# Kernel optimization log

Measured on AMD Instinct MI355X. Metric: run time of the kernel, lower is better.

The kernel has to match this reference:

```python
import jax, jax.numpy as jnp
import numpy as np

B, H, E = 16, 4096, 512
N_MODES = 24  # len(index_q), permutation of range(48//2)


def setup_inputs() -> dict:
    key = jax.random.key(0)
    ks = jax.random.split(key, 7)
    s = 1.0 / np.sqrt(E)
    inp = {
        "x": jax.random.normal(ks[0], (B, H, E), jnp.float32),
        "Wq": jax.random.normal(ks[1], (E, E), jnp.float32) * s,
        "bq": jax.random.normal(ks[2], (E,), jnp.float32) * s,
        "Wk": jax.random.normal(ks[3], (E, E), jnp.float32) * s,
        "bk": jax.random.normal(ks[4], (E,), jnp.float32) * s,
        "Wv": jax.random.normal(ks[5], (E, E), jnp.float32) * s,
        "bv": jax.random.normal(ks[6], (E,), jnp.float32) * s,
        # shuffled permutation of range(24), as in the module __init__
        "index_q": jnp.asarray(np.random.RandomState(0).permutation(N_MODES), jnp.int32),
    }
    return inp


def reference(x, Wq, bq, Wk, bk, Wv, bv, index_q):
    # nn.Linear: y = x @ W.T + b
    Q = x @ Wq.T + bq
    K = x @ Wk.T + bk
    V = x @ Wv.T + bv  # computed but unused downstream (faithful to original bug)
    del V

    # rFFT over feature dim, gather selected frequency modes (vectorized,
    # replacing the original per-index Python loops)
    xq_ft = jnp.fft.rfft(Q, axis=-1)[:, :, index_q]          # [B,H,24] complex
    xk_ft = jnp.fft.rfft(K, axis=-1)[:, :, index_q]          # [B,H,24]
    xv_ft = xk_ft                                            # original uses rfft(K) for V too

    # cross-frequency attention: contract over H (no conjugation, as torch.einsum)
    xqk_ft = jnp.einsum('bhx,bhy->bxy', xq_ft, xk_ft)        # [B,24,24] complex
    att = jax.nn.softmax(jnp.abs(xqk_ft), axis=-1)           # real [B,24,24]
    att_c = jax.lax.complex(att, jnp.zeros_like(att))
    xqkv_ft = jnp.einsum('bxy,bhy->bhx', att_c, xv_ft)       # [B,H,24]

    # scatter selected modes back into the full spectrum, inverse rFFT
    n_freq = E // 2 + 1
    out_ft = jnp.zeros((x.shape[0], x.shape[1], n_freq), jnp.complex64)
    out_ft = out_ft.at[:, :, index_q].set(xqkv_ft)
    out = jnp.fft.irfft(out_ft, n=E, axis=-1)                # [B,H,E] real
    return out.astype(x.dtype)
```

## Files before the change

### kernel.cpp

```cpp
#include <hip/hip_runtime.h>
#include <stdint.h>

#define E_DIM 512
#define NM 24
#define NC 48
#define NCOL 96
#define B_DIM 16
#define H_DIM 4096
#define NROWS (B_DIM * H_DIM)

typedef _Float16 half8 __attribute__((ext_vector_type(8)));
typedef float f32x4 __attribute__((ext_vector_type(4)));

__global__ __launch_bounds__(128)
void k_build(const float* __restrict__ Wq, const float* __restrict__ Wk,
             const float* __restrict__ bq, const float* __restrict__ bk,
             const int* __restrict__ idxq,
             _Float16* __restrict__ Cth, _Float16* __restrict__ Ctl,
             float* __restrict__ dvec, float* __restrict__ M) {
  __shared__ float twc[E_DIM], tws[E_DIM];
  __shared__ int fj[NM];
  const int t = threadIdx.x;
  const int bid = blockIdx.x;
  if (bid >= E_DIM + 1) {
    const int gid = (bid - (E_DIM + 1)) * 128 + t;
    const int c = gid >> 9;
    const int e = gid & (E_DIM - 1);
    const int j = c >> 1, p = c & 1;
    const int f = idxq[j];
    const float w = (f == 0 ? 1.0f : 2.0f) * (1.0f / (float)E_DIM);
    float s, cc;
    sincospif((float)((f * e) & (E_DIM - 1)) * (1.0f / 256.0f), &s, &cc);
    M[c * E_DIM + e] = p ? (-w * s) : (w * cc);
    return;
  }
  for (int i = t; i < E_DIM; i += 128) {
    float s, c;
    sincospif((float)i * (1.0f / 256.0f), &s, &c);
    twc[i] = c; tws[i] = s;
  }
  if (t < NM) fj[t] = idxq[t];
  __syncthreads();
  const int e = bid;
  if (t >= NCOL) return;
  const int mat = t / NC;
  const int c = t - mat * NC;
  const int j = c >> 1, p = c & 1;
  const int f = fj[j];
  float acc = 0.0f;
  if (e < E_DIM) {
    const float* __restrict__ W = mat ? Wk : Wq;
    for (int o = 0; o < E_DIM; ++o) {
      const float w = W[o * E_DIM + e];
      const int tt = (f * o) & (E_DIM - 1);
      acc = fmaf(w, p ? -tws[tt] : twc[tt], acc);
    }
    const _Float16 hi = (_Float16)acc;
    Cth[t * E_DIM + e] = hi;
    Ctl[t * E_DIM + e] = (_Float16)(acc - (float)hi);
  } else {
    const float* __restrict__ bv = mat ? bk : bq;
    for (int o = 0; o < E_DIM; ++o) {
      const int tt = (f * o) & (E_DIM - 1);
      acc = fmaf(bv[o], p ? -tws[tt] : twc[tt], acc);
    }
    dvec[t] = acc;
  }
}

__global__ __launch_bounds__(256)
void k_gemmG(const float* __restrict__ x, const _Float16* __restrict__ Cth,
             const _Float16* __restrict__ Ctl, const float* __restrict__ dvec,
             float* __restrict__ G, float* __restrict__ Gk) {
  const int t = threadIdx.x;
  const int lane = t & 63;
  const int wv = t >> 6;
  const int rb = blockIdx.x * 256 + wv * 64;
  const int lm = lane & 15;
  const int lk = lane >> 4;
  f32x4 acc[6][4];
#pragma unroll
  for (int mt = 0; mt < 6; ++mt)
#pragma unroll
    for (int nt = 0; nt < 4; ++nt) acc[mt][nt] = (f32x4){0.f, 0.f, 0.f, 0.f};

  for (int k0 = 0; k0 < E_DIM; k0 += 32) {
    half8 xh[4], xl[4];
#pragma unroll
    for (int nt = 0; nt < 4; ++nt) {
      const float* __restrict__ xp =
          &x[(size_t)(rb + nt * 16 + lm) * E_DIM + k0 + lk * 8];
      const float4 v0 = *(const float4*)xp;
      const float4 v1 = *(const float4*)(xp + 4);
      const float vv[8] = {v0.x, v0.y, v0.z, v0.w, v1.x, v1.y, v1.z, v1.w};
#pragma unroll
      for (int i = 0; i < 8; ++i) {
        const _Float16 h = (_Float16)vv[i];
        xh[nt][i] = h;
        xl[nt][i] = (_Float16)(vv[i] - (float)h);
      }
    }
#pragma unroll
    for (int mt = 0; mt < 6; ++mt) {
      const int arow = mt * 16 + lm;
      const half8 Ah = *(const half8*)&Cth[arow * E_DIM + k0 + lk * 8];
      const half8 Al = *(const half8*)&Ctl[arow * E_DIM + k0 + lk * 8];
#pragma unroll
      for (int nt = 0; nt < 4; ++nt) {
        acc[mt][nt] = __builtin_amdgcn_mfma_f32_16x16x32_f16(Ah, xh[nt], acc[mt][nt], 0, 0, 0);
        acc[mt][nt] = __builtin_amdgcn_mfma_f32_16x16x32_f16(Al, xh[nt], acc[mt][nt], 0, 0, 0);
        acc[mt][nt] = __builtin_amdgcn_mfma_f32_16x16x32_f16(Ah, xl[nt], acc[mt][nt], 0, 0, 0);
      }
    }
  }
#pragma unroll
  for (int mt = 0; mt < 6; ++mt) {
    const int c0 = mt * 16 + lk * 4;
    const float4 bias = *(const float4*)&dvec[c0];
#pragma unroll
    for (int nt = 0; nt < 4; ++nt) {
      const int r = rb + nt * 16 + lm;
      float4 st;
      st.x = acc[mt][nt][0] + bias.x;
      st.y = acc[mt][nt][1] + bias.y;
      st.z = acc[mt][nt][2] + bias.z;
      st.w = acc[mt][nt][3] + bias.w;
      *(float4*)&G[(size_t)r * NCOL + c0] = st;
      if (mt >= 3)
        *(float4*)&Gk[(size_t)r * NC + (c0 - NC)] = st;
    }
  }
}

__global__ __launch_bounds__(576)
void k_spart(const float* __restrict__ G, float* __restrict__ Sp) {
  __shared__ __align__(16) float gs[128 * NCOL];
  const int t = threadIdx.x;
  const int xx = t / NM, yy = t - xx * NM;
  const int bc = blockIdx.x;
  const int b = bc >> 5, hc = bc & 31;
  const int r0 = b * H_DIM + hc * 128;
  const float4* __restrict__ g4 = (const float4*)G;
#pragma unroll
  for (int r = 0; r < 6; ++r) {
    const int idx = t + r * 576;
    if (idx < 128 * NCOL / 4)
      ((float4*)gs)[idx] = g4[(size_t)r0 * (NCOL / 4) + idx];
  }
  __syncthreads();
  float sre = 0.0f, sim = 0.0f;
  for (int h = 0; h < 128; ++h) {
    const float2 q = *(const float2*)&gs[h * NCOL + 2 * xx];
    const float2 k = *(const float2*)&gs[h * NCOL + NC + 2 * yy];
    sre += q.x * k.x - q.y * k.y;
    sim += q.x * k.y + q.y * k.x;
  }
  ((float2*)Sp)[bc * 576 + t] = make_float2(sre, sim);
}

__global__ __launch_bounds__(576)
void k_att(const float* __restrict__ Sp, float* __restrict__ att) {
  __shared__ float mag[576];
  __shared__ float ex[576];
  const int t = threadIdx.x;
  const int b = blockIdx.x;
  float sre = 0.0f, sim = 0.0f;
  const float2* in2 = (const float2*)Sp;
  for (int hc = 0; hc < 32; ++hc) {
    const float2 v = in2[(b * 32 + hc) * 576 + t];
    sre += v.x; sim += v.y;
  }
  mag[t] = sqrtf(sre * sre + sim * sim);
  __syncthreads();
  const int xx = t / NM;
  float m = -1e30f;
  for (int k = 0; k < NM; ++k) m = fmaxf(m, mag[xx * NM + k]);
  const float e = expf(mag[t] - m);
  ex[t] = e;
  __syncthreads();
  float s = 0.0f;
  for (int k = 0; k < NM; ++k) s += ex[xx * NM + k];
  att[b * 576 + t] = e / s;
}

#define ZOB 128
#define ZON 256
__global__ __launch_bounds__(512)
void k_zout(const float* __restrict__ Gk, const float* __restrict__ M,
            const float* __restrict__ att, float* __restrict__ out) {
  __shared__ __align__(16) float ms[NC * ZON];
  __shared__ __align__(16) float zs[NC][ZOB + 4];
  __shared__ float at[576];
  const int t = threadIdx.x;
  const int row0 = (blockIdx.x >> 1) * ZOB;
  const int e0 = (blockIdx.x & 1) * ZON;
  const int b = row0 >> 12;
  float4 mv[6];
#pragma unroll
  for (int r = 0; r < 6; ++r) {
    const int idx = r * 512 + t;
    const int k = idx >> 6, ec = idx & 63;
    mv[r] = *(const float4*)&M[k * E_DIM + e0 + ec * 4];
  }
  at[t] = att[b * 576 + t];
  if (t < 64) at[512 + t] = att[b * 576 + 512 + t];
  __syncthreads();
#pragma unroll
  for (int r = 0; r < 6; ++r) {
    const int idx = r * 512 + t;
    *(float4*)&ms[idx * 4] = mv[r];
  }
  const int zrow = t >> 2;
  const int xg = t & 3;
  float gk[NC];
  {
    const float4* gk4 = (const float4*)&Gk[(size_t)(row0 + zrow) * NC];
#pragma unroll
    for (int i = 0; i < 12; ++i) {
      const float4 v = gk4[i];
      gk[i * 4 + 0] = v.x; gk[i * 4 + 1] = v.y;
      gk[i * 4 + 2] = v.z; gk[i * 4 + 3] = v.w;
    }
  }
  float z[12];
#pragma unroll
  for (int j = 0; j < 6; ++j) {
    const int xx = xg * 6 + j;
    float zr = 0.0f, zi = 0.0f;
#pragma unroll
    for (int y = 0; y < NM; ++y) {
      const float a = at[xx * NM + y];
      zr = fmaf(a, gk[2 * y], zr);
      zi = fmaf(a, gk[2 * y + 1], zi);
    }
    z[2 * j] = zr; z[2 * j + 1] = zi;
  }
#pragma unroll
  for (int s = 0; s < 12; ++s) zs[xg * 12 + s][zrow] = z[s];
  __syncthreads();
  const int rr = t >> 4;
  const int cg = t & 15;
  float acc[4][16];
#pragma unroll
  for (int a = 0; a < 4; ++a)
#pragma unroll
    for (int c = 0; c < 16; ++c) acc[a][c] = 0.0f;
#pragma unroll 4
  for (int kk = 0; kk < NC; ++kk) {
    const float4 zv = *(const float4*)&zs[kk][rr * 4];
    const float4 m0 = *(const float4*)&ms[kk * ZON + cg * 8 + 0];
    const float4 m1 = *(const float4*)&ms[kk * ZON + cg * 8 + 4];
    const float4 m2 = *(const float4*)&ms[kk * ZON + cg * 8 + 128];
    const float4 m3 = *(const float4*)&ms[kk * ZON + cg * 8 + 132];
    const float zr[4] = {zv.x, zv.y, zv.z, zv.w};
    const float mr[16] = {m0.x, m0.y, m0.z, m0.w, m1.x, m1.y, m1.z, m1.w,
                          m2.x, m2.y, m2.z, m2.w, m3.x, m3.y, m3.z, m3.w};
#pragma unroll
    for (int a = 0; a < 4; ++a)
#pragma unroll
      for (int c = 0; c < 16; ++c)
        acc[a][c] = fmaf(zr[a], mr[c], acc[a][c]);
  }
#pragma unroll
  for (int a = 0; a < 4; ++a) {
    const int row = row0 + rr * 4 + a;
    float4 v0, v1, v2, v3;
    v0.x = acc[a][0];  v0.y = acc[a][1];  v0.z = acc[a][2];  v0.w = acc[a][3];
    v1.x = acc[a][4];  v1.y = acc[a][5];  v1.z = acc[a][6];  v1.w = acc[a][7];
    v2.x = acc[a][8];  v2.y = acc[a][9];  v2.z = acc[a][10]; v2.w = acc[a][11];
    v3.x = acc[a][12]; v3.y = acc[a][13]; v3.z = acc[a][14]; v3.w = acc[a][15];
    float* o = &out[(size_t)row * E_DIM + e0 + cg * 8];
    *(float4*)(o + 0)   = v0;
    *(float4*)(o + 4)   = v1;
    *(float4*)(o + 128) = v2;
    *(float4*)(o + 132) = v3;
  }
}

extern "C" void kernel_launch(void* const* d_in, const int* in_sizes, int n_in,
                              void* d_out, int out_size, void* d_ws, size_t ws_size,
                              hipStream_t stream) {
  const float* x  = (const float*)d_in[0];
  const float* Wq = (const float*)d_in[1];
  const float* bq = (const float*)d_in[2];
  const float* Wk = (const float*)d_in[3];
  const float* bk = (const float*)d_in[4];
  const int* idxq = (const int*)d_in[7];
  float* out = (float*)d_out;
  float* ws = (float*)d_ws;

  _Float16* Cth = (_Float16*)ws;
  _Float16* Ctl = (_Float16*)(ws + 24576);
  float* dv  = ws + 49152;
  float* M   = ws + 49280;
  float* att = ws + 73856;
  float* Sp  = ws + 83072;
  float* Gk  = ws + 672896;
  float* G   = out;

  k_build<<<E_DIM + 1 + (NC * E_DIM) / 128, 128, 0, stream>>>(Wq, Wk, bq, bk, idxq, Cth, Ctl, dv, M);
  k_gemmG<<<NROWS / 256, 256, 0, stream>>>(x, Cth, Ctl, dv, G, Gk);
  k_spart<<<B_DIM * 32, 576, 0, stream>>>(G, Sp);
  k_att<<<B_DIM, 576, 0, stream>>>(Sp, att);
  k_zout<<<(NROWS / ZOB) * (E_DIM / ZON), 512, 0, stream>>>(Gk, M, att, out);
}
```

Baseline: 405.1 us.

## Fuse partial cross-spectrum reduction into GEMM epilogue and restructure build kernel

The per-chunk Q·K cross-frequency partial sums are now computed inside the projection GEMM kernel: the accumulators are staged through shared memory in two halves and reduced over the block's 256 rows. This removes the full Q/K spectrum write to global memory and the separate k_spart kernel that read it back. k_build is also reorganised so each block owns one output column, with a coalesced W read, a per-block twiddle table and a wave-shuffle bias reduction. The cost is extra LDS use and syncs in the GEMM epilogue, with 576 pairs spread over 256 threads, which may reduce occupancy.

```diff
diff --git a/kernel.cpp b/kernel.cpp
--- a/kernel.cpp
+++ b/kernel.cpp
@@ -8,70 +8,69 @@
 #define B_DIM 16
 #define H_DIM 4096
 #define NROWS (B_DIM * H_DIM)
+#define NPAIR 576
 
 typedef _Float16 half8 __attribute__((ext_vector_type(8)));
 typedef float f32x4 __attribute__((ext_vector_type(4)));
 
-__global__ __launch_bounds__(128)
+__global__ __launch_bounds__(512)
 void k_build(const float* __restrict__ Wq, const float* __restrict__ Wk,
              const float* __restrict__ bq, const float* __restrict__ bk,
              const int* __restrict__ idxq,
              _Float16* __restrict__ Cth, _Float16* __restrict__ Ctl,
              float* __restrict__ dvec, float* __restrict__ M) {
-  __shared__ float twc[E_DIM], tws[E_DIM];
-  __shared__ int fj[NM];
   const int t = threadIdx.x;
   const int bid = blockIdx.x;
-  if (bid >= E_DIM + 1) {
-    const int gid = (bid - (E_DIM + 1)) * 128 + t;
-    const int c = gid >> 9;
-    const int e = gid & (E_DIM - 1);
+  if (bid >= NCOL) {
+    const int c = bid - NCOL;
     const int j = c >> 1, p = c & 1;
     const int f = idxq[j];
     const float w = (f == 0 ? 1.0f : 2.0f) * (1.0f / (float)E_DIM);
     float s, cc;
-    sincospif((float)((f * e) & (E_DIM - 1)) * (1.0f / 256.0f), &s, &cc);
-    M[c * E_DIM + e] = p ? (-w * s) : (w * cc);
+    sincospif((float)((f * t) & (E_DIM - 1)) * (1.0f / 256.0f), &s, &cc);
+    M[c * E_DIM + t] = p ? (-w * s) : (w * cc);
     return;
   }
-  for (int i = t; i < E_DIM; i += 128) {
-    float s, c;
-    sincospif((float)i * (1.0f / 256.0f), &s, &c);
-    twc[i] = c; tws[i] = s;
-  }
-  if (t < NM) fj[t] = idxq[t];
-  __syncthreads();
-  const int e = bid;
-  if (t >= NCOL) return;
-  const int mat = t / NC;
-  const int c = t - mat * NC;
+  __shared__ float tw[E_DIM];
+  const int mat = bid / NC;
+  const int c = bid - mat * NC;
   const int j = c >> 1, p = c & 1;
-  const int f = fj[j];
+  const int f = idxq[j];
+  {
+    float s, cc;
+    sincospif((float)((f * t) & (E_DIM - 1)) * (1.0f / 256.0f), &s, &cc);
+    tw[t] = p ? -s : cc;
+  }
+  __syncthreads();
+  const float* __restrict__ W = mat ? Wk : Wq;
   float acc = 0.0f;
-  if (e < E_DIM) {
-    const float* __restrict__ W = mat ? Wk : Wq;
-    for (int o = 0; o < E_DIM; ++o) {
-      const float w = W[o * E_DIM + e];
-      const int tt = (f * o) & (E_DIM - 1);
-      acc = fmaf(w, p ? -tws[tt] : twc[tt], acc);
-    }
-    const _Float16 hi = (_Float16)acc;
-    Cth[t * E_DIM + e] = hi;
-    Ctl[t * E_DIM + e] = (_Float16)(acc - (float)hi);
-  } else {
+#pragma unroll 8
+  for (int o = 0; o < E_DIM; ++o)
+    acc = fmaf(W[o * E_DIM + t], tw[o], acc);
+  const _Float16 hi = (_Float16)acc;
+  Cth[bid * E_DIM + t] = hi;
+  Ctl[bid * E_DIM + t] = (_Float16)(acc - (float)hi);
+  if (t < 64) {
     const float* __restrict__ bv = mat ? bk : bq;
-    for (int o = 0; o < E_DIM; ++o) {
-      const int tt = (f * o) & (E_DIM - 1);
-      acc = fmaf(bv[o], p ? -tws[tt] : twc[tt], acc);
-    }
-    dvec[t] = acc;
-  }
-}
-
+    float ba = 0.0f;
+#pragma unroll
+    for (int r = 0; r < 8; ++r) {
+      const int o = r * 64 + t;
+      ba = fmaf(bv[o], tw[o], ba);
+    }
+#pragma unroll
+    for (int off = 32; off > 0; off >>= 1)
+      ba += __shfl_down(ba, off, 64);
+    if (t == 0) dvec[bid] = ba;
+  }
+}
+
+#define GSTR 100
 __global__ __launch_bounds__(256)
 void k_gemmG(const float* __restrict__ x, const _Float16* __restrict__ Cth,
              const _Float16* __restrict__ Ctl, const float* __restrict__ dvec,
-             float* __restrict__ G, float* __restrict__ Gk) {
+             float* __restrict__ Gk, float* __restrict__ Sp) {
+  __shared__ __align__(16) float gs[128 * GSTR];
   const int t = threadIdx.x;
   const int lane = t & 63;
   const int wv = t >> 6;
@@ -119,55 +118,72 @@
     const float4 bias = *(const float4*)&dvec[c0];
 #pragma unroll
     for (int nt = 0; nt < 4; ++nt) {
-      const int r = rb + nt * 16 + lm;
-      float4 st;
-      st.x = acc[mt][nt][0] + bias.x;
-      st.y = acc[mt][nt][1] + bias.y;
-      st.z = acc[mt][nt][2] + bias.z;
-      st.w = acc[mt][nt][3] + bias.w;
-      *(float4*)&G[(size_t)r * NCOL + c0] = st;
-      if (mt >= 3)
+      acc[mt][nt][0] += bias.x;
+      acc[mt][nt][1] += bias.y;
+      acc[mt][nt][2] += bias.z;
+      acc[mt][nt][3] += bias.w;
+      if (mt >= 3) {
+        const int r = rb + nt * 16 + lm;
+        float4 st;
+        st.x = acc[mt][nt][0]; st.y = acc[mt][nt][1];
+        st.z = acc[mt][nt][2]; st.w = acc[mt][nt][3];
         *(float4*)&Gk[(size_t)r * NC + (c0 - NC)] = st;
-    }
-  }
-}
-
-__global__ __launch_bounds__(576)
-void k_spart(const float* __restrict__ G, float* __restrict__ Sp) {
-  __shared__ __align__(16) float gs[128 * NCOL];
-  const int t = threadIdx.x;
-  const int xx = t / NM, yy = t - xx * NM;
-  const int bc = blockIdx.x;
-  const int b = bc >> 5, hc = bc & 31;
-  const int r0 = b * H_DIM + hc * 128;
-  const float4* __restrict__ g4 = (const float4*)G;
-#pragma unroll
-  for (int r = 0; r < 6; ++r) {
-    const int idx = t + r * 576;
-    if (idx < 128 * NCOL / 4)
-      ((float4*)gs)[idx] = g4[(size_t)r0 * (NCOL / 4) + idx];
-  }
-  __syncthreads();
-  float sre = 0.0f, sim = 0.0f;
-  for (int h = 0; h < 128; ++h) {
-    const float2 q = *(const float2*)&gs[h * NCOL + 2 * xx];
-    const float2 k = *(const float2*)&gs[h * NCOL + NC + 2 * yy];
-    sre += q.x * k.x - q.y * k.y;
-    sim += q.x * k.y + q.y * k.x;
-  }
-  ((float2*)Sp)[bc * 576 + t] = make_float2(sre, sim);
+      }
+    }
+  }
+  float sre[3] = {0.f, 0.f, 0.f}, sim[3] = {0.f, 0.f, 0.f};
+#pragma unroll
+  for (int half = 0; half < 2; ++half) {
+    __syncthreads();
+    if ((wv >> 1) == half) {
+#pragma unroll
+      for (int mt = 0; mt < 6; ++mt) {
+        const int c0 = mt * 16 + lk * 4;
+#pragma unroll
+        for (int nt = 0; nt < 4; ++nt) {
+          const int lrow = (wv & 1) * 64 + nt * 16 + lm;
+          float4 st;
+          st.x = acc[mt][nt][0]; st.y = acc[mt][nt][1];
+          st.z = acc[mt][nt][2]; st.w = acc[mt][nt][3];
+          *(float4*)&gs[lrow * GSTR + c0] = st;
+        }
+      }
+    }
+    __syncthreads();
+#pragma unroll
+    for (int r = 0; r < 3; ++r) {
+      const int i = t + r * 256;
+      if (i < NPAIR) {
+        const int xx = i / NM, yy = i - xx * NM;
+        float ar = 0.f, ai = 0.f;
+        for (int h = 0; h < 128; ++h) {
+          const float2 q = *(const float2*)&gs[h * GSTR + 2 * xx];
+          const float2 k = *(const float2*)&gs[h * GSTR + NC + 2 * yy];
+          ar += q.x * k.x - q.y * k.y;
+          ai += q.x * k.y + q.y * k.x;
+        }
+        sre[r] += ar; sim[r] += ai;
+      }
+    }
+  }
+#pragma unroll
+  for (int r = 0; r < 3; ++r) {
+    const int i = t + r * 256;
+    if (i < NPAIR)
+      ((float2*)Sp)[(size_t)blockIdx.x * NPAIR + i] = make_float2(sre[r], sim[r]);
+  }
 }
 
 __global__ __launch_bounds__(576)
 void k_att(const float* __restrict__ Sp, float* __restrict__ att) {
-  __shared__ float mag[576];
-  __shared__ float ex[576];
+  __shared__ float mag[NPAIR];
+  __shared__ float ex[NPAIR];
   const int t = threadIdx.x;
   const int b = blockIdx.x;
   float sre = 0.0f, sim = 0.0f;
   const float2* in2 = (const float2*)Sp;
-  for (int hc = 0; hc < 32; ++hc) {
-    const float2 v = in2[(b * 32 + hc) * 576 + t];
+  for (int hc = 0; hc < 16; ++hc) {
+    const float2 v = in2[(size_t)(b * 16 + hc) * NPAIR + t];
     sre += v.x; sim += v.y;
   }
   mag[t] = sqrtf(sre * sre + sim * sim);
@@ -180,7 +196,7 @@
   __syncthreads();
   float s = 0.0f;
   for (int k = 0; k < NM; ++k) s += ex[xx * NM + k];
-  att[b * 576 + t] = e / s;
+  att[b * NPAIR + t] = e / s;
 }
 
 #define ZOB 128
@@ -190,7 +206,7 @@
             const float* __restrict__ att, float* __restrict__ out) {
   __shared__ __align__(16) float ms[NC * ZON];
   __shared__ __align__(16) float zs[NC][ZOB + 4];
-  __shared__ float at[576];
+  __shared__ float at[NPAIR];
   const int t = threadIdx.x;
   const int row0 = (blockIdx.x >> 1) * ZOB;
   const int e0 = (blockIdx.x & 1) * ZON;
@@ -202,8 +218,8 @@
     const int k = idx >> 6, ec = idx & 63;
     mv[r] = *(const float4*)&M[k * E_DIM + e0 + ec * 4];
   }
-  at[t] = att[b * 576 + t];
-  if (t < 64) at[512 + t] = att[b * 576 + 512 + t];
+  at[t] = att[b * NPAIR + t];
+  if (t < 64) at[512 + t] = att[b * NPAIR + 512 + t];
   __syncthreads();
 #pragma unroll
   for (int r = 0; r < 6; ++r) {
@@ -295,12 +311,10 @@
   float* M   = ws + 49280;
   float* att = ws + 73856;
   float* Sp  = ws + 83072;
-  float* Gk  = ws + 672896;
-  float* G   = out;
-
-  k_build<<<E_DIM + 1 + (NC * E_DIM) / 128, 128, 0, stream>>>(Wq, Wk, bq, bk, idxq, Cth, Ctl, dv, M);
-  k_gemmG<<<NROWS / 256, 256, 0, stream>>>(x, Cth, Ctl, dv, G, Gk);
-  k_spart<<<B_DIM * 32, 576, 0, stream>>>(G, Sp);
+  float* Gk  = ws + 377984;
+
+  k_build<<<NCOL + NC, 512, 0, stream>>>(Wq, Wk, bq, bk, idxq, Cth, Ctl, dv, M);
+  k_gemmG<<<NROWS / 256, 256, 0, stream>>>(x, Cth, Ctl, dv, Gk, Sp);
   k_att<<<B_DIM, 576, 0, stream>>>(Sp, att);
   k_zout<<<(NROWS / ZOB) * (E_DIM / ZON), 512, 0, stream>>>(Gk, M, att, out);
 }
```

Measured after the change: 357.9 us. 11.6% less time.
